# Performance work log

Hardware: AMD Instinct MI355X
Metric: run time of the kernel (lower is better)

Reference implementation:

```python
import jax, jax.numpy as jnp
import numpy as np

DT = 0.04  # CFG.dt in the original repo (Euler step for FitzHugh-Nagumo)


def _fhn_scan(z, dt):
    """Integrate FitzHugh-Nagumo dynamics over time.
    z: (B, T, N) input current per timestep. Returns V: (B, T, N), with V[:,0]=0.
    V[k] = (1+dt)V[k-1] - dt/3 V[k-1]^3 - dt S[k-1] + dt z[k-1]
    S[k] = S[k-1] + dt*0.08*(V[k-1] + 0.7 - 0.8 S[k-1])
    """
    B, T, N = z.shape
    z_t = jnp.transpose(z, (1, 0, 2))  # (T, B, N), time-major for scan

    def step(carry, z_prev):
        V, S = carry
        Vn = (1.0 + dt) * V - (dt / 3.0) * (V ** 3) - dt * S + dt * z_prev
        Sn = S + dt * 0.08 * (V + 0.7 - 0.8 * S)
        return (Vn, Sn), Vn

    init = (jnp.zeros((B, N), z.dtype), jnp.zeros((B, N), z.dtype))
    _, Vs = jax.lax.scan(step, init, z_t[:-1])  # (T-1, B, N): V[1:]
    V = jnp.concatenate([jnp.zeros((1, B, N), z.dtype), Vs], axis=0)
    return jnp.transpose(V, (1, 0, 2))  # (B, T, N)


def setup_inputs() -> dict:
    key = jax.random.key(0)
    k1, k2, k3 = jax.random.split(key, 3)
    B, T = 64, 2048
    batch = jax.random.normal(k1, (B, T, 784), dtype=jnp.float32)
    # nn.Linear default init: U(-1/sqrt(fan_in), 1/sqrt(fan_in))
    W1 = jax.random.uniform(k2, (100, 784), jnp.float32, -1.0, 1.0) / np.sqrt(784.0)
    W2 = jax.random.uniform(k3, (10, 100), jnp.float32, -1.0, 1.0) / np.sqrt(100.0)
    return {"batch": batch, "W1": W1, "W2": W2}


def reference(batch, W1, W2):
    dt = DT
    z1 = jnp.einsum('btd,nd->btn', batch, W1)  # (B, T, 100)
    V1 = _fhn_scan(z1, dt)                      # (B, T, 100)
    z2 = jnp.einsum('btn,mn->btm', V1 * 0.5, W2)  # (B, T, 10)
    V2 = _fhn_scan(z2, dt)                      # (B, T, 10)
    return V2
```

## Files before the change

### kernel.cpp

```cpp
#include <hip/hip_runtime.h>
#include <hip/hip_bf16.h>


#define FHN_DT 0.04f

typedef _Float16 f16x8 __attribute__((ext_vector_type(8)));
typedef __attribute__((ext_vector_type(4))) float          f32x4;
typedef __attribute__((ext_vector_type(8))) unsigned short ushort8;

__device__ __forceinline__ void sync_lds() {
    asm volatile("s_waitcnt lgkmcnt(0)" ::: "memory");
    __builtin_amdgcn_s_barrier();
    asm volatile("" ::: "memory");
}

__global__ void prep_w3(const float* __restrict__ W1, unsigned short* __restrict__ Wg) {
    int idx = blockIdx.x * 256 + threadIdx.x;
    if (idx >= 224000) return;
    int sh    = idx % 40;
    int rest  = idx / 40;
    int n     = rest % 112;
    int rest2 = rest / 112;
    int term  = rest2 % 2;
    int kt    = rest2 / 2;
    int k = kt * 32 + sh;
    float v = (n < 100 && sh < 32 && k < 784) ? W1[n * 784 + k] : 0.0f;
    _Float16 h = (_Float16)v;
    _Float16 l = (_Float16)((v - (float)h) * 1024.0f);
    Wg[idx] = (term == 0) ? __builtin_bit_cast(unsigned short, h)
                          : __builtin_bit_cast(unsigned short, l);
}

#define GW_TILE 8960

__global__ __launch_bounds__(256, 2) void gemm1_n(const float* __restrict__ A,
                                                  const unsigned short* __restrict__ Wg,
                                                  float* __restrict__ z1p) {
    __shared__ __align__(16) unsigned short Wl[2][GW_TILE];
    const int tid  = threadIdx.x;
    const int w    = tid >> 6;
    const int lane = tid & 63;
    const int ln   = lane & 15;
    const int kg   = lane >> 4;
    const long row0 = (long)blockIdx.x * 128;

    const float* arow0 = A + (row0 + w * 32 + ln) * 784 + kg * 8;
    const float* arow1 = arow0 + (size_t)16 * 784;

    f32x4 acc1[2][7] = {};
    f32x4 acc2[2][7] = {};
    float afpA[16], afpB[16];
    ushort8 wreg[5];

#define ISSUE_A(T, AF) {                                                        \
        if ((T) == 24 && kg >= 2) {                                             \
            *(float4*)&AF[0]  = make_float4(0.f, 0.f, 0.f, 0.f);                \
            *(float4*)&AF[4]  = make_float4(0.f, 0.f, 0.f, 0.f);                \
            *(float4*)&AF[8]  = make_float4(0.f, 0.f, 0.f, 0.f);                \
            *(float4*)&AF[12] = make_float4(0.f, 0.f, 0.f, 0.f);                \
        } else {                                                                \
            *(float4*)&AF[0]  = *(const float4*)(arow0 + (T) * 32);             \
            *(float4*)&AF[4]  = *(const float4*)(arow0 + (T) * 32 + 4);         \
            *(float4*)&AF[8]  = *(const float4*)(arow1 + (T) * 32);             \
            *(float4*)&AF[12] = *(const float4*)(arow1 + (T) * 32 + 4);         \
        } }

#define LOADW(T) {                                                              \
        _Pragma("unroll")                                                       \
        for (int j_ = 0; j_ < 5; ++j_) {                                        \
            int off_ = j_ * 4096 + tid * 16;                                    \
            if (off_ < 17920)                                                   \
                wreg[j_] = *(const ushort8*)((const char*)Wg                    \
                            + (size_t)(T) * 17920 + off_);                      \
        } }

#define BODY(KT, AF) {                                                          \
                       \
        f16x8 ah0, al0, ah1, al1;                                               \
        _Pragma("unroll")                                                       \
        for (int e_ = 0; e_ < 8; ++e_) {                                        \
            float a0_ = AF[e_], a1_ = AF[8 + e_];                               \
            _Float16 h0_ = (_Float16)a0_, h1_ = (_Float16)a1_;                  \
            ah0[e_] = h0_; ah1[e_] = h1_;                                       \
            al0[e_] = (_Float16)((a0_ - (float)h0_) * 1024.0f);                 \
            al1[e_] = (_Float16)((a1_ - (float)h1_) * 1024.0f);                 \
        }                                                                       \
             \
        {                                                                       \
            unsigned short* buf_ = &Wl[(KT) & 1][0];                            \
            _Pragma("unroll")                                                   \
            for (int j_ = 0; j_ < 5; ++j_) {                                    \
                int off_ = j_ * 4096 + tid * 16;                                \
                if (off_ < 17920) *(ushort8*)((char*)buf_ + off_) = wreg[j_];   \
            }                                                                   \
        }                                                                       \
                     \
        if ((KT) < 24) LOADW((KT) + 1);                                         \
        if ((KT) < 23) ISSUE_A((KT) + 2, AF);                                   \
                            \
        sync_lds();                                                             \
                   \
        const unsigned short* cb_ = &Wl[(KT) & 1][0];                           \
        _Pragma("unroll")                                                       \
        for (int ct_ = 0; ct_ < 7; ++ct_) {                                     \
            const unsigned short* pw_ = cb_ + (ct_ * 16 + ln) * 40 + kg * 8;    \
            f16x8 bh = *(const f16x8*)(pw_);                                    \
            f16x8 bl = *(const f16x8*)(pw_ + 4480);                             \
            acc1[0][ct_] = __builtin_amdgcn_mfma_f32_16x16x32_f16(ah0, bh, acc1[0][ct_], 0, 0, 0); \
            acc2[0][ct_] = __builtin_amdgcn_mfma_f32_16x16x32_f16(ah0, bl, acc2[0][ct_], 0, 0, 0); \
            acc2[0][ct_] = __builtin_amdgcn_mfma_f32_16x16x32_f16(al0, bh, acc2[0][ct_], 0, 0, 0); \
            acc1[1][ct_] = __builtin_amdgcn_mfma_f32_16x16x32_f16(ah1, bh, acc1[1][ct_], 0, 0, 0); \
            acc2[1][ct_] = __builtin_amdgcn_mfma_f32_16x16x32_f16(ah1, bl, acc2[1][ct_], 0, 0, 0); \
            acc2[1][ct_] = __builtin_amdgcn_mfma_f32_16x16x32_f16(al1, bh, acc2[1][ct_], 0, 0, 0); \
        } }

    LOADW(0);
    ISSUE_A(0, afpA);
    ISSUE_A(1, afpB);

    for (int kt2 = 0; kt2 < 12; ++kt2) {
        BODY(kt2 * 2,     afpA);
        BODY(kt2 * 2 + 1, afpB);
    }
    BODY(24, afpA);

#pragma unroll
    for (int ct = 0; ct < 7; ++ct) {
        int n = ct * 16 + ln;
        if (n < 100) {
#pragma unroll
            for (int rt = 0; rt < 2; ++rt) {
                long rg = row0 + w * 32 + rt * 16 + kg * 4;
                float* p = z1p + rg * 100 + n;
#pragma unroll
                for (int r = 0; r < 4; ++r)
                    p[r * 100] = fmaf(acc2[rt][ct][r], 0.0009765625f, acc1[rt][ct][r]);
            }
        }
    }
#undef ISSUE_A
#undef LOADW
#undef BODY
}

__global__ __launch_bounds__(512) void fused_scan(const float* __restrict__ z1p,
                                                  const float* __restrict__ W2,
                                                  float* __restrict__ out) {
    __shared__ float fsm[32768];
    const int tid = threadIdx.x;
    const int b   = blockIdx.x;
    const float dt = FHN_DT;

    float V = 0.f, S = 0.f;
    const float* zb = z1p + (long)b * 2048 * 100 + tid;
    float z0[16], z1r[16], z2r[16], z3r[16];
    if (tid < 100) {
#pragma unroll
        for (int u = 0; u < 16; ++u) {
            z0[u]  = zb[u * 100];
            z1r[u] = zb[(16 + u) * 100];
            z2r[u] = zb[(32 + u) * 100];
            z3r[u] = zb[(48 + u) * 100];
        }
    }

    const int tg = tid - 128;
    int pp = tg >> 7;
    pp = __builtin_amdgcn_readfirstlane(pp);
    const int r  = tg & 127;
    const int mb = (pp == 0) ? 0 : (pp == 1 ? 4 : 7);
    const int mc = (pp == 0) ? 4 : 3;

    for (int i = 0; i <= 18; ++i) {
        if (tid < 128) {
            bool a1 = (tid < 100) && (i < 16);
            bool a2 = (tid >= 100) && (tid < 110) && (i >= 2) && (i < 18);
            if (a1 || a2) {
                const int cw = i & 1;
#pragma unroll
                for (int sub = 0; sub < 8; ++sub) {
                    float zt[16];
                    if (a1) {
                        int tn = (i * 8 + sub + 4) * 16;
                        if (tn < 2048) {
#pragma unroll
                            for (int u = 0; u < 16; ++u) zt[u] = zb[(tn + u) * 100];
                        }
                    }
                    if (a2) {
#pragma unroll
                        for (int u = 0; u < 16; ++u)
                            z0[u] = fsm[29696 + cw * 1536 + (sub * 16 + u) * 12 + (tid - 100)];
                    }
#pragma unroll
                    for (int u = 0; u < 16; ++u) {
                        int tl = sub * 16 + u;
                        fsm[cw * 14848 + tl * 116 + tid] = V;
                        float z  = z0[u];
                        float V3 = V * V * V;
                        float Vn = fmaf(1.f + dt, V,
                                    fmaf(-dt / 3.f, V3, fmaf(-dt, S, dt * z)));
                        float Sn = fmaf(dt * 0.08f, V + 0.7f - 0.8f * S, S);
                        V = Vn; S = Sn;
                    }
                    if (a1) {
#pragma unroll
                        for (int u = 0; u < 16; ++u) {
                            z0[u] = z1r[u]; z1r[u] = z2r[u]; z2r[u] = z3r[u]; z3r[u] = zt[u];
                        }
                    }
                }
            }
        } else {
            if (i >= 1 && i <= 16) {
                const int pb = (i - 1) & 1;
                float acc[4] = {0.f, 0.f, 0.f, 0.f};
                for (int kq = 0; kq < 25; ++kq) {
                    float4 v = *(const float4*)&fsm[pb * 14848 + r * 116 + kq * 4];
#pragma unroll
                    for (int j = 0; j < 4; ++j) {
                        if (j < mc) {
                            const float* wp = W2 + (mb + j) * 100 + kq * 4;
                            acc[j] = fmaf(v.x, wp[0], acc[j]);
                            acc[j] = fmaf(v.y, wp[1], acc[j]);
                            acc[j] = fmaf(v.z, wp[2], acc[j]);
                            acc[j] = fmaf(v.w, wp[3], acc[j]);
                        }
                    }
                }
#pragma unroll
                for (int j = 0; j < 4; ++j)
                    if (j < mc) fsm[29696 + pb * 1536 + r * 12 + mb + j] = 0.5f * acc[j];
            }
            if (i >= 3) {
                const int pb = (i - 1) & 1;
                float* dst = out + ((long)b * 2048 + (long)(i - 3) * 128 + r) * 10;
#pragma unroll
                for (int j = 0; j < 4; ++j)
                    if (j < mc) dst[mb + j] = fsm[pb * 14848 + r * 116 + 100 + mb + j];
            }
        }
        sync_lds();
    }
}

extern "C" void kernel_launch(void* const* d_in, const int* in_sizes, int n_in,
                              void* d_out, int out_size, void* d_ws, size_t ws_size,
                              hipStream_t stream) {
    const float* batch = (const float*)d_in[0];
    const float* W1    = (const float*)d_in[1];
    const float* W2    = (const float*)d_in[2];
    float* out = (float*)d_out;

    char* base = (char*)d_ws;
    unsigned short* Wg = (unsigned short*)base;
    float* z1p = (float*)(base + 448000);

    prep_w3<<<875, 256, 0, stream>>>(W1, Wg);
    gemm1_n<<<1024, 256, 0, stream>>>(batch, Wg, z1p);
    fused_scan<<<64, 512, 0, stream>>>(z1p, W2, out);
}
```

Before: 221.5 us.

## Split first FHN scan into separate kernel spread over more blocks

The layer-1 FitzHugh-Nagumo scan moves out of the 64-block fused kernel into its own kernel, one thread per (batch, neuron) channel across 50 blocks, and writes V1 to workspace. The fused kernel now streams V1 tiles from global memory into LDS and runs only the matmul-2 and layer-2 scan stages. The goal is to spread the serial 2048-step scan over more CUs instead of 100 lanes per block on 64 blocks. In exchange it adds a kernel launch and a full write and re-read of V1 through global memory, and the new scan kernel still fills only 50 blocks.

```diff
diff --git a/kernel.cpp b/kernel.cpp
--- a/kernel.cpp
+++ b/kernel.cpp
@@ -75,7 +75,6 @@
         } }
 
 #define BODY(KT, AF) {                                                          \
-                       \
         f16x8 ah0, al0, ah1, al1;                                               \
         _Pragma("unroll")                                                       \
         for (int e_ = 0; e_ < 8; ++e_) {                                        \
@@ -85,7 +84,6 @@
             al0[e_] = (_Float16)((a0_ - (float)h0_) * 1024.0f);                 \
             al1[e_] = (_Float16)((a1_ - (float)h1_) * 1024.0f);                 \
         }                                                                       \
-             \
         {                                                                       \
             unsigned short* buf_ = &Wl[(KT) & 1][0];                            \
             _Pragma("unroll")                                                   \
@@ -94,12 +92,9 @@
                 if (off_ < 17920) *(ushort8*)((char*)buf_ + off_) = wreg[j_];   \
             }                                                                   \
         }                                                                       \
-                     \
         if ((KT) < 24) LOADW((KT) + 1);                                         \
         if ((KT) < 23) ISSUE_A((KT) + 2, AF);                                   \
-                            \
         sync_lds();                                                             \
-                   \
         const unsigned short* cb_ = &Wl[(KT) & 1][0];                           \
         _Pragma("unroll")                                                       \
         for (int ct_ = 0; ct_ < 7; ++ct_) {                                     \
@@ -143,26 +138,55 @@
 #undef BODY
 }
 
-__global__ __launch_bounds__(512) void fused_scan(const float* __restrict__ z1p,
-                                                  const float* __restrict__ W2,
-                                                  float* __restrict__ out) {
+__global__ __launch_bounds__(128) void scan1_k(const float* __restrict__ z1p,
+                                               float* __restrict__ V1) {
+    int c = blockIdx.x * 128 + threadIdx.x;
+    if (c >= 6400) return;
+    int b = c / 100, n = c % 100;
+    const float dt = FHN_DT;
+    const float* zb = z1p + (long)b * 204800 + n;
+    float* vb = V1 + (long)b * 204800 + n;
+    float V = 0.f, S = 0.f;
+    float z0[16], z1r[16], z2r[16], z3r[16];
+#pragma unroll
+    for (int u = 0; u < 16; ++u) {
+        z0[u]  = zb[u * 100];
+        z1r[u] = zb[(16 + u) * 100];
+        z2r[u] = zb[(32 + u) * 100];
+        z3r[u] = zb[(48 + u) * 100];
+    }
+    for (int g = 0; g < 128; ++g) {
+        float zt[16];
+        int tn = (g + 4) * 16;
+        if (tn < 2048) {
+#pragma unroll
+            for (int u = 0; u < 16; ++u) zt[u] = zb[(tn + u) * 100];
+        }
+#pragma unroll
+        for (int u = 0; u < 16; ++u) {
+            vb[(g * 16 + u) * 100] = V;
+            float z  = z0[u];
+            float V3 = V * V * V;
+            float Vn = fmaf(1.f + dt, V,
+                        fmaf(-dt / 3.f, V3, fmaf(-dt, S, dt * z)));
+            float Sn = fmaf(dt * 0.08f, V + 0.7f - 0.8f * S, S);
+            V = Vn; S = Sn;
+        }
+#pragma unroll
+        for (int u = 0; u < 16; ++u) {
+            z0[u] = z1r[u]; z1r[u] = z2r[u]; z2r[u] = z3r[u]; z3r[u] = zt[u];
+        }
+    }
+}
+
+__global__ __launch_bounds__(512) void fused2(const float* __restrict__ V1,
+                                              const float* __restrict__ W2,
+                                              float* __restrict__ out) {
     __shared__ float fsm[32768];
     const int tid = threadIdx.x;
     const int b   = blockIdx.x;
     const float dt = FHN_DT;
-
     float V = 0.f, S = 0.f;
-    const float* zb = z1p + (long)b * 2048 * 100 + tid;
-    float z0[16], z1r[16], z2r[16], z3r[16];
-    if (tid < 100) {
-#pragma unroll
-        for (int u = 0; u < 16; ++u) {
-            z0[u]  = zb[u * 100];
-            z1r[u] = zb[(16 + u) * 100];
-            z2r[u] = zb[(32 + u) * 100];
-            z3r[u] = zb[(48 + u) * 100];
-        }
-    }
 
     const int tg = tid - 128;
     int pp = tg >> 7;
@@ -173,45 +197,39 @@
 
     for (int i = 0; i <= 18; ++i) {
         if (tid < 128) {
-            bool a1 = (tid < 100) && (i < 16);
             bool a2 = (tid >= 100) && (tid < 110) && (i >= 2) && (i < 18);
-            if (a1 || a2) {
+            if (a2) {
                 const int cw = i & 1;
 #pragma unroll
                 for (int sub = 0; sub < 8; ++sub) {
-                    float zt[16];
-                    if (a1) {
-                        int tn = (i * 8 + sub + 4) * 16;
-                        if (tn < 2048) {
-#pragma unroll
-                            for (int u = 0; u < 16; ++u) zt[u] = zb[(tn + u) * 100];
-                        }
-                    }
-                    if (a2) {
-#pragma unroll
-                        for (int u = 0; u < 16; ++u)
-                            z0[u] = fsm[29696 + cw * 1536 + (sub * 16 + u) * 12 + (tid - 100)];
-                    }
+                    float z0s[16];
+#pragma unroll
+                    for (int u = 0; u < 16; ++u)
+                        z0s[u] = fsm[29696 + cw * 1536 + (sub * 16 + u) * 12 + (tid - 100)];
 #pragma unroll
                     for (int u = 0; u < 16; ++u) {
                         int tl = sub * 16 + u;
                         fsm[cw * 14848 + tl * 116 + tid] = V;
-                        float z  = z0[u];
+                        float z  = z0s[u];
                         float V3 = V * V * V;
                         float Vn = fmaf(1.f + dt, V,
                                     fmaf(-dt / 3.f, V3, fmaf(-dt, S, dt * z)));
                         float Sn = fmaf(dt * 0.08f, V + 0.7f - 0.8f * S, S);
                         V = Vn; S = Sn;
                     }
-                    if (a1) {
-#pragma unroll
-                        for (int u = 0; u < 16; ++u) {
-                            z0[u] = z1r[u]; z1r[u] = z2r[u]; z2r[u] = z3r[u]; z3r[u] = zt[u];
-                        }
-                    }
                 }
             }
         } else {
+            float4 sreg[9];
+            const bool st = (i < 16);
+            if (st) {
+                const float* src = V1 + (long)b * 204800 + (long)i * 12800;
+#pragma unroll
+                for (int j = 0; j < 9; ++j) {
+                    int f = j * 384 + tg;
+                    if (f < 3200) sreg[j] = *(const float4*)(src + f * 4);
+                }
+            }
             if (i >= 1 && i <= 16) {
                 const int pb = (i - 1) & 1;
                 float acc[4] = {0.f, 0.f, 0.f, 0.f};
@@ -232,6 +250,17 @@
                 for (int j = 0; j < 4; ++j)
                     if (j < mc) fsm[29696 + pb * 1536 + r * 12 + mb + j] = 0.5f * acc[j];
             }
+            if (st) {
+                const int cw = i & 1;
+#pragma unroll
+                for (int j = 0; j < 9; ++j) {
+                    int f = j * 384 + tg;
+                    if (f < 3200) {
+                        int rr = f / 25, c4 = f % 25;
+                        *(float4*)&fsm[cw * 14848 + rr * 116 + c4 * 4] = sreg[j];
+                    }
+                }
+            }
             if (i >= 3) {
                 const int pb = (i - 1) & 1;
                 float* dst = out + ((long)b * 2048 + (long)(i - 3) * 128 + r) * 10;
@@ -255,8 +284,10 @@
     char* base = (char*)d_ws;
     unsigned short* Wg = (unsigned short*)base;
     float* z1p = (float*)(base + 448000);
+    float* V1  = z1p + (size_t)131072 * 100;
 
     prep_w3<<<875, 256, 0, stream>>>(W1, Wg);
     gemm1_n<<<1024, 256, 0, stream>>>(batch, Wg, z1p);
-    fused_scan<<<64, 512, 0, stream>>>(z1p, W2, out);
-}
+    scan1_k<<<50, 128, 0, stream>>>(z1p, V1);
+    fused2<<<64, 512, 0, stream>>>(V1, W2, out);
+}
```

Measured after the change: 319.9 us. 44.4% more time.

## Move layer-2 FHN scan to a dedicated wavefront to avoid divergence

Applied to the files above, without the earlier changes.

The second-layer scan previously ran on lanes 100-109 of the same wavefront as the first-layer scan lanes, so the two divergent paths serialized. A ninth wavefront (block size 576) now runs the layer-2 scan on its own and reads its inputs from shared memory. This is meant to let both scans proceed concurrently, at the cost of an extra wave per block.

```diff
diff --git a/kernel.cpp b/kernel.cpp
--- a/kernel.cpp
+++ b/kernel.cpp
@@ -75,7 +75,6 @@
         } }
 
 #define BODY(KT, AF) {                                                          \
-                       \
         f16x8 ah0, al0, ah1, al1;                                               \
         _Pragma("unroll")                                                       \
         for (int e_ = 0; e_ < 8; ++e_) {                                        \
@@ -85,7 +84,6 @@
             al0[e_] = (_Float16)((a0_ - (float)h0_) * 1024.0f);                 \
             al1[e_] = (_Float16)((a1_ - (float)h1_) * 1024.0f);                 \
         }                                                                       \
-             \
         {                                                                       \
             unsigned short* buf_ = &Wl[(KT) & 1][0];                            \
             _Pragma("unroll")                                                   \
@@ -94,12 +92,9 @@
                 if (off_ < 17920) *(ushort8*)((char*)buf_ + off_) = wreg[j_];   \
             }                                                                   \
         }                                                                       \
-                     \
         if ((KT) < 24) LOADW((KT) + 1);                                         \
         if ((KT) < 23) ISSUE_A((KT) + 2, AF);                                   \
-                            \
         sync_lds();                                                             \
-                   \
         const unsigned short* cb_ = &Wl[(KT) & 1][0];                           \
         _Pragma("unroll")                                                       \
         for (int ct_ = 0; ct_ < 7; ++ct_) {                                     \
@@ -143,9 +138,9 @@
 #undef BODY
 }
 
-__global__ __launch_bounds__(512) void fused_scan(const float* __restrict__ z1p,
-                                                  const float* __restrict__ W2,
-                                                  float* __restrict__ out) {
+__global__ __launch_bounds__(576) void fused_scan3(const float* __restrict__ z1p,
+                                                   const float* __restrict__ W2,
+                                                   float* __restrict__ out) {
     __shared__ float fsm[32768];
     const int tid = threadIdx.x;
     const int b   = blockIdx.x;
@@ -165,33 +160,26 @@
     }
 
     const int tg = tid - 128;
-    int pp = tg >> 7;
+    int pp = (tg >> 7) & 3;
     pp = __builtin_amdgcn_readfirstlane(pp);
     const int r  = tg & 127;
     const int mb = (pp == 0) ? 0 : (pp == 1 ? 4 : 7);
     const int mc = (pp == 0) ? 4 : 3;
+    const int m2 = tid - 512;
 
     for (int i = 0; i <= 18; ++i) {
         if (tid < 128) {
             bool a1 = (tid < 100) && (i < 16);
-            bool a2 = (tid >= 100) && (tid < 110) && (i >= 2) && (i < 18);
-            if (a1 || a2) {
-                const int cw = i & 1;
+            if (a1) {
 #pragma unroll
                 for (int sub = 0; sub < 8; ++sub) {
                     float zt[16];
-                    if (a1) {
-                        int tn = (i * 8 + sub + 4) * 16;
-                        if (tn < 2048) {
-#pragma unroll
-                            for (int u = 0; u < 16; ++u) zt[u] = zb[(tn + u) * 100];
-                        }
-                    }
-                    if (a2) {
-#pragma unroll
-                        for (int u = 0; u < 16; ++u)
-                            z0[u] = fsm[29696 + cw * 1536 + (sub * 16 + u) * 12 + (tid - 100)];
-                    }
+                    int tn = (i * 8 + sub + 4) * 16;
+                    if (tn < 2048) {
+#pragma unroll
+                        for (int u = 0; u < 16; ++u) zt[u] = zb[(tn + u) * 100];
+                    }
+                    const int cw = i & 1;
 #pragma unroll
                     for (int u = 0; u < 16; ++u) {
                         int tl = sub * 16 + u;
@@ -203,15 +191,13 @@
                         float Sn = fmaf(dt * 0.08f, V + 0.7f - 0.8f * S, S);
                         V = Vn; S = Sn;
                     }
-                    if (a1) {
-#pragma unroll
-                        for (int u = 0; u < 16; ++u) {
-                            z0[u] = z1r[u]; z1r[u] = z2r[u]; z2r[u] = z3r[u]; z3r[u] = zt[u];
-                        }
+#pragma unroll
+                    for (int u = 0; u < 16; ++u) {
+                        z0[u] = z1r[u]; z1r[u] = z2r[u]; z2r[u] = z3r[u]; z3r[u] = zt[u];
                     }
                 }
             }
-        } else {
+        } else if (tid < 512) {
             if (i >= 1 && i <= 16) {
                 const int pb = (i - 1) & 1;
                 float acc[4] = {0.f, 0.f, 0.f, 0.f};
@@ -239,6 +225,29 @@
                 for (int j = 0; j < 4; ++j)
                     if (j < mc) dst[mb + j] = fsm[pb * 14848 + r * 116 + 100 + mb + j];
             }
+        } else {
+            bool a2 = (m2 < 10) && (i >= 2) && (i < 18);
+            if (a2) {
+                const int cw = i & 1;
+#pragma unroll
+                for (int sub = 0; sub < 8; ++sub) {
+                    float z0s[16];
+#pragma unroll
+                    for (int u = 0; u < 16; ++u)
+                        z0s[u] = fsm[29696 + cw * 1536 + (sub * 16 + u) * 12 + m2];
+#pragma unroll
+                    for (int u = 0; u < 16; ++u) {
+                        int tl = sub * 16 + u;
+                        fsm[cw * 14848 + tl * 116 + 100 + m2] = V;
+                        float z  = z0s[u];
+                        float V3 = V * V * V;
+                        float Vn = fmaf(1.f + dt, V,
+                                    fmaf(-dt / 3.f, V3, fmaf(-dt, S, dt * z)));
+                        float Sn = fmaf(dt * 0.08f, V + 0.7f - 0.8f * S, S);
+                        V = Vn; S = Sn;
+                    }
+                }
+            }
         }
         sync_lds();
     }
@@ -258,5 +267,5 @@
 
     prep_w3<<<875, 256, 0, stream>>>(W1, Wg);
     gemm1_n<<<1024, 256, 0, stream>>>(batch, Wg, z1p);
-    fused_scan<<<64, 512, 0, stream>>>(z1p, W2, out);
-}
+    fused_scan3<<<64, 576, 0, stream>>>(z1p, W2, out);
+}
```

New measurement: 204.3 us. 7.8% less time.
